# Performance work log

Hardware: AMD Instinct MI355X
Metric: run time of the kernel (lower is better)

Reference implementation:

```python
import jax, jax.numpy as jnp
import numpy as np

SEQ, BATCH = 256, 8
N_NODES = SEQ * BATCH
VOCAB, D_MODEL, H, D_K, D_FF, N_LAYERS, MAX_POS = 259, 256, 8, 32, 1024, 2, 128


def setup_inputs() -> dict:
    key = jax.random.key(0)
    ks = jax.random.split(key, 16)
    # structured causal edge list per sequence (dst attends to src <= dst, incl. self)
    tri_dst, tri_src = np.tril_indices(SEQ)
    offs = (np.arange(BATCH) * SEQ)[:, None]
    edge_src = jnp.asarray((tri_src[None, :] + offs).ravel(), dtype=jnp.int64)
    edge_dst = jnp.asarray((tri_dst[None, :] + offs).ravel(), dtype=jnp.int64)
    positions = jnp.tile(jnp.arange(SEQ, dtype=jnp.int64), BATCH)
    tokens = jax.random.randint(ks[0], (N_NODES,), 0, VOCAB, dtype=jnp.int64)
    s = 0.02
    p = lambda k, shp: jax.random.normal(k, shp, dtype=jnp.float32) * s
    return {
        "tokens": tokens, "positions": positions,
        "edge_src": edge_src, "edge_dst": edge_dst,
        "coord_emb": p(ks[1], (3, D_MODEL)),
        "pos_emb": p(ks[2], (MAX_POS, D_MODEL)),
        "value_emb": p(ks[3], (VOCAB, D_MODEL)),
        "ln1_scale": jnp.ones((N_LAYERS, D_MODEL)), "ln1_bias": jnp.zeros((N_LAYERS, D_MODEL)),
        "Wqkv": p(ks[4], (N_LAYERS, D_MODEL, 3 * D_MODEL)),
        "Wo": p(ks[5], (N_LAYERS, D_MODEL, D_MODEL)),
        "ln2_scale": jnp.ones((N_LAYERS, D_MODEL)), "ln2_bias": jnp.zeros((N_LAYERS, D_MODEL)),
        "W1": p(ks[6], (N_LAYERS, D_MODEL, D_FF)), "b1": jnp.zeros((N_LAYERS, D_FF)),
        "W2": p(ks[7], (N_LAYERS, D_FF, D_MODEL)), "b2": jnp.zeros((N_LAYERS, D_MODEL)),
        "lnf_scale": jnp.ones((D_MODEL,)), "lnf_bias": jnp.zeros((D_MODEL,)),
        "Wg": p(ks[8], (D_MODEL, VOCAB)), "bg": jnp.zeros((VOCAB,)),
    }


def _ln(x, scale, bias, eps=1e-5):
    mu = jnp.mean(x, axis=-1, keepdims=True)
    var = jnp.var(x, axis=-1, keepdims=True)
    return (x - mu) * jax.lax.rsqrt(var + eps) * scale + bias


def _graph_attention(x, src, dst, Wqkv, Wo, ln_s, ln_b):
    n = x.shape[0]
    xn = _ln(x, ln_s, ln_b)
    qkv = (xn @ Wqkv).reshape(n, 3, H, D_K)
    q, k, v = qkv[:, 0], qkv[:, 1], qkv[:, 2]  # [n, H, D_K] each
    # u_dot_v('k','q','score') per edge, scaled
    score = jnp.einsum("ehd,ehd->eh", k[src], q[dst]) / jnp.sqrt(jnp.float32(D_K))
    # edge_softmax over incoming edges of each dst node
    smax = jax.ops.segment_max(score, dst, num_segments=n)      # [n, H]
    ex = jnp.exp(score - smax[dst])                              # [E, H]
    denom = jax.ops.segment_sum(ex, dst, num_segments=n)        # [n, H]
    alpha = ex / denom[dst]
    # u_mul_e('v','softmax_score') + sum reduce -> z on dst nodes
    z = jax.ops.segment_sum(alpha[:, :, None] * v[src], dst, num_segments=n)  # [n, H, D_K]
    return x + z.reshape(n, D_MODEL) @ Wo


def reference(tokens, positions, edge_src, edge_dst, coord_emb, pos_emb, value_emb,
              ln1_scale, ln1_bias, Wqkv, Wo, ln2_scale, ln2_bias, W1, b1, W2, b2,
              lnf_scale, lnf_bias, Wg, bg):
    x = coord_emb[positions % 3] + pos_emb[positions // 3] + value_emb[tokens]
    for i in range(Wqkv.shape[0]):
        x = _graph_attention(x, edge_src, edge_dst, Wqkv[i], Wo[i], ln1_scale[i], ln1_bias[i])
        h = _ln(x, ln2_scale[i], ln2_bias[i])
        x = x + jax.nn.relu(h @ W1[i] + b1[i]) @ W2[i] + b2[i]
    out = _ln(x, lnf_scale, lnf_bias) @ Wg + bg
    return jax.nn.log_softmax(out, axis=-1)
```

## Files before the change

### kernel.cpp

```cpp
#include <hip/hip_runtime.h>
#include <hip/hip_bf16.h>

typedef __hip_bfloat16 bf16;
typedef unsigned short ushort_t;
typedef unsigned int uint_t;
typedef __attribute__((ext_vector_type(8))) short short8;
typedef __attribute__((ext_vector_type(4))) float floatx4;

#define D_MODEL 256
#define SEQ     256
#define BATCH   8
#define NN      2048
#define NHEAD   8
#define DK      32
#define DFF     1024
#define VOCAB   259
#define NLAYER  2

#define WQKVT_OFF 0
#define WOT_OFF   393216
#define W1T_OFF   524288
#define W2T_OFF   1048576
#define WGT_OFF   1572864
#define WT_TOTAL  1639168
#define LNP_TOTAL 2560
#define BP_TOTAL  2819

template<bool BF>
__device__ __forceinline__ float ldw(const void* p, int i) {
    if (BF) return __bfloat162float(((const bf16*)p)[i]);
    return ((const float*)p)[i];
}
template<bool BF>
__device__ __forceinline__ ushort_t ldb(const void* p, size_t i) {
    if (BF) return ((const ushort_t*)p)[i];
    bf16 h = __float2bfloat16(((const float*)p)[i]);
    ushort_t u; __builtin_memcpy(&u, &h, 2); return u;
}
template<bool I64>
__device__ __forceinline__ int ldi(const void* p, int i) {
    if (I64) return (int)(((const long long*)p)[i]);
    return ((const int*)p)[i];
}
__device__ __forceinline__ ushort_t f2bs(float f) {
    bf16 h = __float2bfloat16(f);
    ushort_t u; __builtin_memcpy(&u, &h, 2); return u;
}
__device__ __forceinline__ float bs2f(uint_t u16) {
    return __uint_as_float(u16 << 16);
}
__device__ __forceinline__ float wred_sum(float v) {
    #pragma unroll
    for (int m = 32; m > 0; m >>= 1) v += __shfl_xor(v, m, 64);
    return v;
}
__device__ __forceinline__ float wred_max(float v) {
    #pragma unroll
    for (int m = 32; m > 0; m >>= 1) v = fmaxf(v, __shfl_xor(v, m, 64));
    return v;
}
__device__ __forceinline__ bool detBF(const void* ln1s) {
    return *(const uint_t*)ln1s == 0x3F803F80u;
}
__device__ __forceinline__ bool detI64(const void* pos) {
    const int* p32 = (const int*)pos;
    return p32[1] == 0 && p32[2] == 1;
}

template<bool BF>
__device__ void ttile(const void* src, size_t srcOff, int K, int N, int tk, int tn,
                      ushort_t* dst, ushort_t (*tile)[68]) {
    int t = threadIdx.x;
    #pragma unroll
    for (int pass = 0; pass < 16; ++pass) {
        int e = pass * 256 + t;
        int kl = e >> 6, nl = e & 63;
        int n = tn * 64 + nl;
        tile[kl][nl] = (n < N) ? ldb<BF>(src, srcOff + (size_t)(tk*64 + kl) * N + n)
                               : (ushort_t)0;
    }
    __syncthreads();
    #pragma unroll
    for (int pass = 0; pass < 16; ++pass) {
        int e = pass * 256 + t;
        int nl = e >> 6, kl = e & 63;
        int n = tn * 64 + nl;
        if (n < N) dst[(size_t)n * K + tk*64 + kl] = tile[kl][nl];
    }
}

template<bool BF, bool I64>
__device__ void embedln16(const void* tok, const void* pos,
        const void* ce, const void* pe, const void* ve,
        const void* ln1s, const void* ln1b, int rowBase,
        float* x, ushort_t* xn) {
    int lane = threadIdx.x & 63, wave = threadIdx.x >> 6;
    #pragma unroll
    for (int i = 0; i < 4; ++i) {
        int n = rowBase + wave * 4 + i;
        int p  = ldi<I64>(pos, n);
        int tk = ldi<I64>(tok, n);
        int c0 = lane * 4;
        float v[4];
        #pragma unroll
        for (int j = 0; j < 4; ++j)
            v[j] = ldw<BF>(ce, (p % 3) * 256 + c0 + j)
                 + ldw<BF>(pe, (p / 3) * 256 + c0 + j)
                 + ldw<BF>(ve, tk * 256 + c0 + j);
        float s  = wred_sum(v[0] + v[1] + v[2] + v[3]);
        float s2 = wred_sum(v[0]*v[0] + v[1]*v[1] + v[2]*v[2] + v[3]*v[3]);
        float mu = s * (1.f/256.f);
        float var = s2 * (1.f/256.f) - mu * mu;
        float rstd = rsqrtf(var + 1e-5f);
        *reinterpret_cast<float4*>(&x[(size_t)n*256 + c0]) =
            make_float4(v[0], v[1], v[2], v[3]);
        ushort4 o;
        o.x = f2bs((v[0]-mu)*rstd*ldw<BF>(ln1s, c0+0) + ldw<BF>(ln1b, c0+0));
        o.y = f2bs((v[1]-mu)*rstd*ldw<BF>(ln1s, c0+1) + ldw<BF>(ln1b, c0+1));
        o.z = f2bs((v[2]-mu)*rstd*ldw<BF>(ln1s, c0+2) + ldw<BF>(ln1b, c0+2));
        o.w = f2bs((v[3]-mu)*rstd*ldw<BF>(ln1s, c0+3) + ldw<BF>(ln1b, c0+3));
        *reinterpret_cast<ushort4*>(&xn[(size_t)n*256 + c0]) = o;
    }
}

template<bool BF, bool I64>
__device__ void prep_body(const void* tok, const void* pos,
        const void* ce, const void* pe, const void* ve,
        const void* Wqkv, const void* Wo, const void* W1, const void* W2, const void* Wg,
        const void* ln1s, const void* ln1b, const void* ln2s, const void* ln2b,
        const void* lnfs, const void* lnfb,
        const void* b1, const void* b2, const void* bg,
        ushort_t* WT, float* lnP, float* bP, float* x, ushort_t* xn,
        ushort_t (*tile)[68]) {
    int blk = blockIdx.x;
    if (blk < 404) {
        const void* src; int K, N, tk, tn; size_t dstOff, srcOff;
        if (blk < 96)       { int L = blk/48, lo = blk%48; src=Wqkv; K=256; N=768;
                              srcOff=(size_t)L*196608; dstOff=WQKVT_OFF+(size_t)L*196608;
                              tk=lo/12; tn=lo%12; }
        else if (blk < 128) { int b2=blk-96, L=b2/16, lo=b2%16; src=Wo; K=256; N=256;
                              srcOff=(size_t)L*65536; dstOff=WOT_OFF+(size_t)L*65536;
                              tk=lo/4; tn=lo%4; }
        else if (blk < 256) { int b2=blk-128, L=b2/64, lo=b2%64; src=W1; K=256; N=1024;
                              srcOff=(size_t)L*262144; dstOff=W1T_OFF+(size_t)L*262144;
                              tk=lo/16; tn=lo%16; }
        else if (blk < 384) { int b2=blk-256, L=b2/64, lo=b2%64; src=W2; K=1024; N=256;
                              srcOff=(size_t)L*262144; dstOff=W2T_OFF+(size_t)L*262144;
                              tk=lo/4; tn=lo%4; }
        else                { int lo=blk-384; src=Wg; K=256; N=259;
                              srcOff=0; dstOff=WGT_OFF; tk=lo/5; tn=lo%5; }
        ttile<BF>(src, srcOff, K, N, tk, tn, WT + dstOff, tile);
    } else if (blk < 426) {
        int gid = (blk - 404) * 256 + threadIdx.x;
        if (gid < LNP_TOTAL) {
            float v;
            if      (gid < 512)  v = ldw<BF>(ln1s, gid);
            else if (gid < 1024) v = ldw<BF>(ln1b, gid - 512);
            else if (gid < 1536) v = ldw<BF>(ln2s, gid - 1024);
            else if (gid < 2048) v = ldw<BF>(ln2b, gid - 1536);
            else if (gid < 2304) v = ldw<BF>(lnfs, gid - 2048);
            else                 v = ldw<BF>(lnfb, gid - 2304);
            lnP[gid] = v;
        } else if (gid < LNP_TOTAL + BP_TOTAL) {
            int g = gid - LNP_TOTAL;
            float v;
            if      (g < 2048) v = ldw<BF>(b1, g);
            else if (g < 2560) v = ldw<BF>(b2, g - 2048);
            else               v = ldw<BF>(bg, g - 2560);
            bP[g] = v;
        }
    } else {
        embedln16<BF, I64>(tok, pos, ce, pe, ve, ln1s, ln1b, (blk - 426) * 16, x, xn);
    }
}

__global__ void __launch_bounds__(256) prep_k(const void* tok, const void* pos,
        const void* ce, const void* pe, const void* ve,
        const void* Wqkv, const void* Wo, const void* W1, const void* W2, const void* Wg,
        const void* ln1s, const void* ln1b, const void* ln2s, const void* ln2b,
        const void* lnfs, const void* lnfb,
        const void* b1, const void* b2, const void* bg,
        ushort_t* WT, float* lnP, float* bP, float* x, ushort_t* xn) {
    __shared__ ushort_t tile[64][68];
    bool BF = detBF(ln1s), I64 = detI64(pos);
    if (BF) { if (I64) prep_body<true,true >(tok,pos,ce,pe,ve,Wqkv,Wo,W1,W2,Wg,ln1s,ln1b,ln2s,ln2b,lnfs,lnfb,b1,b2,bg,WT,lnP,bP,x,xn,tile);
              else     prep_body<true,false>(tok,pos,ce,pe,ve,Wqkv,Wo,W1,W2,Wg,ln1s,ln1b,ln2s,ln2b,lnfs,lnfb,b1,b2,bg,WT,lnP,bP,x,xn,tile); }
    else    { if (I64) prep_body<false,true >(tok,pos,ce,pe,ve,Wqkv,Wo,W1,W2,Wg,ln1s,ln1b,ln2s,ln2b,lnfs,lnfb,b1,b2,bg,WT,lnP,bP,x,xn,tile);
              else     prep_body<false,false>(tok,pos,ce,pe,ve,Wqkv,Wo,W1,W2,Wg,ln1s,ln1b,ln2s,ln2b,lnfs,lnfb,b1,b2,bg,WT,lnP,bP,x,xn,tile); }
}

union AttnSH {
    struct {
        ushort_t Ks[SEQ][40];
        ushort_t Qs[64][40];
    } a;
    ushort_t Ps[64][264];
};
__global__ void __launch_bounds__(256) attn_k(const ushort_t* __restrict__ qkvB,
                                              ushort_t* __restrict__ zB) {
    __shared__ AttnSH u;
    __shared__ ushort_t Vt[32][264];
    int t = threadIdx.x;
    int lane = t & 63, wave = t >> 6;
    int quad = lane >> 4, l16 = lane & 15;
    int tile = blockIdx.x & 3, bh = blockIdx.x >> 2;
    int b = bh >> 3, h = bh & 7;
    int base = b * SEQ;
    int dstBase = tile * 64;
    int tileEnd = (tile + 1) * 64;

    int nV = tileEnd * 4;
    for (int i = t; i < nV; i += 256) {
        int src = i >> 2, g = i & 3;
        const ushort_t* rp = qkvB + (size_t)(base + src) * 768 + h * 32 + g * 8;
        uint4 kv = *reinterpret_cast<const uint4*>(rp + 256);
        *reinterpret_cast<uint4*>(&u.a.Ks[src][g * 8]) = kv;
        uint4 vv = *reinterpret_cast<const uint4*>(rp + 512);
        const ushort_t* vs = (const ushort_t*)&vv;
        #pragma unroll
        for (int j = 0; j < 8; ++j) Vt[g * 8 + j][src] = vs[j];
    }
    {
        int r = t >> 2, g = t & 3;
        uint4 qv = *reinterpret_cast<const uint4*>(
            qkvB + (size_t)(base + dstBase + r) * 768 + h * 32 + g * 8);
        *reinterpret_cast<uint4*>(&u.a.Qs[r][g * 8]) = qv;
    }
    __syncthreads();

    const float scale = 0.17677669529663687f;
    int stLim = tile * 4 + wave;
    int stCnt = stLim + 1;
    short8 qf = *reinterpret_cast<const short8*>(&u.a.Qs[wave * 16 + l16][quad * 8]);
    floatx4 accs[16];
    #pragma unroll
    for (int st = 0; st < 16; ++st) {
        if (st <= stLim) {
            short8 kf = *reinterpret_cast<const short8*>(&u.a.Ks[st * 16 + l16][quad * 8]);
            accs[st] = __builtin_amdgcn_mfma_f32_16x16x32_bf16(qf, kf, (floatx4){0.f,0.f,0.f,0.f}, 0, 0, 0);
        }
    }
    float mrow[4] = {-3e38f, -3e38f, -3e38f, -3e38f};
    #pragma unroll
    for (int st = 0; st < 16; ++st) {
        if (st <= stLim) {
            int srcg = st * 16 + l16;
            #pragma unroll
            for (int r = 0; r < 4; ++r) {
                int dstg = dstBase + wave * 16 + quad * 4 + r;
                float sv = (srcg <= dstg) ? accs[st][r] * scale : -3e38f;
                accs[st][r] = sv;
                mrow[r] = fmaxf(mrow[r], sv);
            }
        }
    }
    #pragma unroll
    for (int mk = 1; mk < 16; mk <<= 1)
        #pragma unroll
        for (int r = 0; r < 4; ++r) mrow[r] = fmaxf(mrow[r], __shfl_xor(mrow[r], mk, 64));
    float lrow[4] = {0.f, 0.f, 0.f, 0.f};
    #pragma unroll
    for (int st = 0; st < 16; ++st) {
        if (st <= stLim) {
            #pragma unroll
            for (int r = 0; r < 4; ++r) {
                float p = __expf(accs[st][r] - mrow[r]);
                accs[st][r] = p;
                lrow[r] += p;
            }
        }
    }
    #pragma unroll
    for (int mk = 1; mk < 16; mk <<= 1)
        #pragma unroll
        for (int r = 0; r < 4; ++r) lrow[r] += __shfl_xor(lrow[r], mk, 64);
    __syncthreads();

    #pragma unroll
    for (int st = 0; st < 16; ++st) {
        if (st <= stLim) {
            #pragma unroll
            for (int r = 0; r < 4; ++r)
                u.Ps[wave * 16 + quad * 4 + r][st * 16 + l16] = f2bs(accs[st][r]);
        }
    }
    if (stCnt & 1) {
        #pragma unroll
        for (int r = 0; r < 4; ++r)
            u.Ps[wave * 16 + quad * 4 + r][stCnt * 16 + l16] = 0;
    }
    __syncthreads();

    int ktCnt = (stCnt + 1) >> 1;
    floatx4 acco[2];
    acco[0] = (floatx4){0.f,0.f,0.f,0.f};
    acco[1] = (floatx4){0.f,0.f,0.f,0.f};
    #pragma unroll
    for (int kt = 0; kt < 8; ++kt) {
        if (kt < ktCnt) {
            short8 pf = *reinterpret_cast<const short8*>(&u.Ps[wave * 16 + l16][kt * 32 + quad * 8]);
            #pragma unroll
            for (int dn = 0; dn < 2; ++dn) {
                short8 vf = *reinterpret_cast<const short8*>(&Vt[dn * 16 + l16][kt * 32 + quad * 8]);
                acco[dn] = __builtin_amdgcn_mfma_f32_16x16x32_bf16(pf, vf, acco[dn], 0, 0, 0);
            }
        }
    }
    #pragma unroll
    for (int dn = 0; dn < 2; ++dn)
        #pragma unroll
        for (int r = 0; r < 4; ++r)
            zB[(size_t)(base + dstBase + wave * 16 + quad * 4 + r) * 256
               + h * 32 + dn * 16 + l16] = f2bs(acco[dn][r] / lrow[r]);
}

__global__ void __launch_bounds__(256) gemm_k(const ushort_t* __restrict__ A, int K,
        const ushort_t* __restrict__ BT, const float* __restrict__ bias,
        ushort_t* __restrict__ C, int ldc, int relu) {
    int t = threadIdx.x;
    int lane = t & 63, wave = t >> 6;
    int quad = lane >> 4, l16 = lane & 15;
    int wm = (wave >> 1) * 32, wn = (wave & 1) * 32;
    int rowBase = blockIdx.x * 64, colBase = blockIdx.y * 64;
    floatx4 acc[2][2];
    #pragma unroll
    for (int a = 0; a < 2; ++a)
        #pragma unroll
        for (int b = 0; b < 2; ++b) acc[a][b] = (floatx4){0.f,0.f,0.f,0.f};
    const ushort_t* a0 = A + (size_t)(rowBase + wm + l16) * K + quad * 8;
    const ushort_t* a1 = a0 + (size_t)16 * K;
    const ushort_t* b0 = BT + (size_t)(colBase + wn + l16) * K + quad * 8;
    const ushort_t* b1 = b0 + (size_t)16 * K;
    #pragma unroll 8
    for (int k0 = 0; k0 < K; k0 += 32) {
        short8 af0 = *reinterpret_cast<const short8*>(a0 + k0);
        short8 af1 = *reinterpret_cast<const short8*>(a1 + k0);
        short8 bf0 = *reinterpret_cast<const short8*>(b0 + k0);
        short8 bf1 = *reinterpret_cast<const short8*>(b1 + k0);
        acc[0][0] = __builtin_amdgcn_mfma_f32_16x16x32_bf16(af0, bf0, acc[0][0], 0,0,0);
        acc[0][1] = __builtin_amdgcn_mfma_f32_16x16x32_bf16(af0, bf1, acc[0][1], 0,0,0);
        acc[1][0] = __builtin_amdgcn_mfma_f32_16x16x32_bf16(af1, bf0, acc[1][0], 0,0,0);
        acc[1][1] = __builtin_amdgcn_mfma_f32_16x16x32_bf16(af1, bf1, acc[1][1], 0,0,0);
    }
    #pragma unroll
    for (int nt = 0; nt < 2; ++nt) {
        int col = colBase + wn + nt*16 + l16;
        float bb = bias ? bias[col] : 0.f;
        #pragma unroll
        for (int mt = 0; mt < 2; ++mt)
            #pragma unroll
            for (int r = 0; r < 4; ++r) {
                int row = rowBase + wm + mt*16 + quad*4 + r;
                float v = acc[mt][nt][r] + bb;
                if (relu) v = fmaxf(v, 0.f);
                C[(size_t)row * ldc + col] = f2bs(v);
            }
    }
}

__global__ void __launch_bounds__(256) gemmresln_k(const ushort_t* __restrict__ A, int K,
        const ushort_t* __restrict__ BT, const float* __restrict__ bias,
        float* __restrict__ x, const float* __restrict__ ls, const float* __restrict__ lb,
        ushort_t* __restrict__ xnG,
        const void* __restrict__ ln1sRaw, const ushort_t* __restrict__ WgT,
        const float* __restrict__ bgP, void* __restrict__ outp, int doLogits) {
    __shared__ float sparts[4][16][256];
    __shared__ ushort_t xnS[16][264];
    float (*Lg)[273] = reinterpret_cast<float (*)[273]>(&sparts[1][0][0]);
    int t = threadIdx.x;
    int lane = t & 63, wave = t >> 6;
    int quad = lane >> 4, l16 = lane & 15;
    int rowBase = blockIdx.x * 16;
    int Kq = K >> 2;
    int wk0 = wave * Kq;

    {
        floatx4 acc[16];
        #pragma unroll
        for (int nt = 0; nt < 16; ++nt) acc[nt] = (floatx4){0.f,0.f,0.f,0.f};
        const ushort_t* a0 = A + (size_t)(rowBase + l16) * K + wk0 + quad * 8;
        for (int k0 = 0; k0 < Kq; k0 += 32) {
            short8 af = *reinterpret_cast<const short8*>(a0 + k0);
            #pragma unroll
            for (int nt = 0; nt < 16; ++nt) {
                short8 bv = *reinterpret_cast<const short8*>(
                    BT + (size_t)(nt*16 + l16) * K + wk0 + k0 + quad * 8);
                acc[nt] = __builtin_amdgcn_mfma_f32_16x16x32_bf16(af, bv, acc[nt], 0,0,0);
            }
        }
        #pragma unroll
        for (int nt = 0; nt < 16; ++nt)
            #pragma unroll
            for (int r = 0; r < 4; ++r)
                sparts[wave][quad*4 + r][nt*16 + l16] = acc[nt][r];
    }
    __syncthreads();
    {
        float* flat0 = &sparts[0][0][0];
        #pragma unroll
        for (int i = 0; i < 16; ++i) {
            int idx = i * 256 + t;
            int row = idx >> 8, col = idx & 255;
            float v = flat0[idx] + (&sparts[1][0][0])[idx]
                    + (&sparts[2][0][0])[idx] + (&sparts[3][0][0])[idx];
            if (bias) v += bias[col];
            v += x[(size_t)(rowBase + row) * 256 + col];
            x[(size_t)(rowBase + row) * 256 + col] = v;
            flat0[idx] = v;
        }
    }
    __syncthreads();
    #pragma unroll
    for (int i = 0; i < 4; ++i) {
        int row = wave*4 + i;
        int c0 = lane * 4;
        float4 vv = *reinterpret_cast<const float4*>(&sparts[0][row][c0]);
        float s  = wred_sum(vv.x + vv.y + vv.z + vv.w);
        float s2 = wred_sum(vv.x*vv.x + vv.y*vv.y + vv.z*vv.z + vv.w*vv.w);
        float mu = s * (1.f/256.f);
        float var = s2 * (1.f/256.f) - mu*mu;
        float rstd = rsqrtf(var + 1e-5f);
        ushort4 o;
        o.x = f2bs((vv.x-mu)*rstd*ls[c0+0] + lb[c0+0]);
        o.y = f2bs((vv.y-mu)*rstd*ls[c0+1] + lb[c0+1]);
        o.z = f2bs((vv.z-mu)*rstd*ls[c0+2] + lb[c0+2]);
        o.w = f2bs((vv.w-mu)*rstd*ls[c0+3] + lb[c0+3]);
        *reinterpret_cast<ushort4*>(&xnG[(size_t)(rowBase+row)*256 + c0]) = o;
        if (doLogits) *reinterpret_cast<ushort4*>(&xnS[row][c0]) = o;
    }
    if (!doLogits) return;
    __syncthreads();
    int cb = wave * 64;
    const ushort_t* a0 = &xnS[l16][quad * 8];
    {
        floatx4 acc[4];
        #pragma unroll
        for (int nt = 0; nt < 4; ++nt) acc[nt] = (floatx4){0.f,0.f,0.f,0.f};
        #pragma unroll
        for (int kc = 0; kc < 8; ++kc) {
            short8 af = *reinterpret_cast<const short8*>(a0 + kc * 32);
            #pragma unroll
            for (int nt = 0; nt < 4; ++nt) {
                short8 bv = *reinterpret_cast<const short8*>(
                    WgT + (size_t)(cb + nt*16 + l16) * 256 + kc*32 + quad*8);
                acc[nt] = __builtin_amdgcn_mfma_f32_16x16x32_bf16(af, bv, acc[nt], 0,0,0);
            }
        }
        __syncthreads();
        #pragma unroll
        for (int nt = 0; nt < 4; ++nt) {
            int col = cb + nt*16 + l16;
            float bb = bgP[col];
            #pragma unroll
            for (int r = 0; r < 4; ++r)
                Lg[quad*4 + r][col] = acc[nt][r] + bb;
        }
    }
    if (wave == 0) {
        floatx4 acc = (floatx4){0.f,0.f,0.f,0.f};
        int n = 256 + l16;
        int nc = (n < VOCAB) ? n : 0;
        const ushort_t* b0 = WgT + (size_t)nc * 256 + quad * 8;
        #pragma unroll
        for (int kc = 0; kc < 8; ++kc) {
            short8 af = *reinterpret_cast<const short8*>(a0 + kc * 32);
            short8 bv = *reinterpret_cast<const short8*>(b0 + kc * 32);
            acc = __builtin_amdgcn_mfma_f32_16x16x32_bf16(af, bv, acc, 0,0,0);
        }
        #pragma unroll
        for (int r = 0; r < 4; ++r)
            Lg[quad*4 + r][256 + l16] = (n < VOCAB) ? (acc[r] + bgP[n]) : -1e30f;
    }
    __syncthreads();
    int outBF = detBF(ln1sRaw) ? 1 : 0;
    #pragma unroll
    for (int i = 0; i < 4; ++i) {
        int row = wave*4 + i;
        float v0 = Lg[row][lane],     v1 = Lg[row][lane+64];
        float v2 = Lg[row][lane+128], v3 = Lg[row][lane+192];
        float v4 = (lane < 16) ? Lg[row][256+lane] : -1e30f;
        float m = wred_max(fmaxf(fmaxf(fmaxf(v0,v1), fmaxf(v2,v3)), v4));
        float se = __expf(v0-m) + __expf(v1-m) + __expf(v2-m) + __expf(v3-m)
                 + ((lane < 16) ? __expf(v4-m) : 0.f);
        se = wred_sum(se);
        float lse = m + logf(se);
        size_t nbase = (size_t)(rowBase + row) * VOCAB;
        if (outBF) {
            ushort_t* o = (ushort_t*)outp + nbase;
            o[lane]     = f2bs(v0 - lse);
            o[lane+64]  = f2bs(v1 - lse);
            o[lane+128] = f2bs(v2 - lse);
            o[lane+192] = f2bs(v3 - lse);
            if (lane < 3) o[256+lane] = f2bs(v4 - lse);
        } else {
            float* o = (float*)outp + nbase;
            o[lane]     = v0 - lse;
            o[lane+64]  = v1 - lse;
            o[lane+128] = v2 - lse;
            o[lane+192] = v3 - lse;
            if (lane < 3) o[256+lane] = v4 - lse;
        }
    }
}

extern "C" void kernel_launch(void* const* d_in, const int* in_sizes, int n_in,
                              void* d_out, int out_size, void* d_ws, size_t ws_size,
                              hipStream_t stream) {
    const void* tok  = d_in[0];
    const void* pos  = d_in[1];
    const void* ce   = d_in[4];
    const void* pe   = d_in[5];
    const void* ve   = d_in[6];
    const void* ln1s = d_in[7];
    const void* ln1b = d_in[8];
    const void* Wqkv = d_in[9];
    const void* Wo   = d_in[10];
    const void* ln2s = d_in[11];
    const void* ln2b = d_in[12];
    const void* W1   = d_in[13];
    const void* b1   = d_in[14];
    const void* W2   = d_in[15];
    const void* b2   = d_in[16];
    const void* lnfs = d_in[17];
    const void* lnfb = d_in[18];
    const void* Wg   = d_in[19];
    const void* bg   = d_in[20];

    char* base = (char*)d_ws;
    float*    lnP  = (float*)base;
    float*    bP   = (float*)(base + 10240);
    float*    x    = (float*)(base + 22528);
    ushort_t* xn   = (ushort_t*)(base + 2119680);
    ushort_t* zB   = (ushort_t*)(base + 3168256);
    ushort_t* ffB  = (ushort_t*)(base + 4216832);
    ushort_t* WT   = (ushort_t*)(base + 8411136);
    ushort_t* qkvB = (ushort_t*)(base + 11689472);

    prep_k<<<554, 256, 0, stream>>>(tok, pos, ce, pe, ve,
        Wqkv, Wo, W1, W2, Wg, ln1s, ln1b, ln2s, ln2b, lnfs, lnfb,
        b1, b2, bg, WT, lnP, bP, x, xn);
    for (int L = 0; L < NLAYER; ++L) {
        gemm_k<<<dim3(32, 12), 256, 0, stream>>>(xn, 256,
            WT + WQKVT_OFF + (size_t)L * 768 * 256, nullptr, qkvB, 768, 0);
        attn_k<<<256, 256, 0, stream>>>(qkvB, zB);
        gemmresln_k<<<128, 256, 0, stream>>>(zB, 256,
            WT + WOT_OFF + (size_t)L * 256 * 256, nullptr,
            x, lnP + 1024 + L * 256, lnP + 1536 + L * 256, xn,
            ln1s, WT + WGT_OFF, bP + 2560, d_out, 0);
        gemm_k<<<dim3(32, 16), 256, 0, stream>>>(xn, 256,
            WT + W1T_OFF + (size_t)L * 1024 * 256, bP + L * 1024, ffB, 1024, 1);
        const float* lsN = (L == 0) ? (lnP + 256)       : (lnP + 2048);
        const float* lbN = (L == 0) ? (lnP + 512 + 256) : (lnP + 2304);
        gemmresln_k<<<128, 256, 0, stream>>>(ffB, 1024,
            WT + W2T_OFF + (size_t)L * 256 * 1024, bP + 2048 + L * 256,
            x, lsN, lbN, xn,
            ln1s, WT + WGT_OFF, bP + 2560, d_out, (L == NLAYER - 1) ? 1 : 0);
    }
}
```

Before: 239.3 us.

## Fuse all stages into a cooperative persistent megakernel with grid syncs

After: 241.6 us. No clear change (+0.9%).

```diff
diff --git a/kernel.cpp b/kernel.cpp
--- a/kernel.cpp
+++ b/kernel.cpp
@@ -1,5 +1,8 @@
 #include <hip/hip_runtime.h>
 #include <hip/hip_bf16.h>
+#include <hip/hip_cooperative_groups.h>
+
+namespace cg = cooperative_groups;
 
 typedef __hip_bfloat16 bf16;
 typedef unsigned short ushort_t;
@@ -26,6 +29,10 @@
 #define LNP_TOTAL 2560
 #define BP_TOTAL  2819
 
+__device__ __forceinline__ ushort_t f2bs(float f) {
+    bf16 h = __float2bfloat16(f);
+    ushort_t u; __builtin_memcpy(&u, &h, 2); return u;
+}
 template<bool BF>
 __device__ __forceinline__ float ldw(const void* p, int i) {
     if (BF) return __bfloat162float(((const bf16*)p)[i]);
@@ -34,20 +41,21 @@
 template<bool BF>
 __device__ __forceinline__ ushort_t ldb(const void* p, size_t i) {
     if (BF) return ((const ushort_t*)p)[i];
-    bf16 h = __float2bfloat16(((const float*)p)[i]);
-    ushort_t u; __builtin_memcpy(&u, &h, 2); return u;
+    return f2bs(((const float*)p)[i]);
 }
 template<bool I64>
 __device__ __forceinline__ int ldi(const void* p, int i) {
     if (I64) return (int)(((const long long*)p)[i]);
     return ((const int*)p)[i];
 }
-__device__ __forceinline__ ushort_t f2bs(float f) {
-    bf16 h = __float2bfloat16(f);
-    ushort_t u; __builtin_memcpy(&u, &h, 2); return u;
-}
-__device__ __forceinline__ float bs2f(uint_t u16) {
-    return __uint_as_float(u16 << 16);
+__device__ __forceinline__ float ldwr(const void* p, int i, bool BF) {
+    return BF ? __bfloat162float(((const bf16*)p)[i]) : ((const float*)p)[i];
+}
+__device__ __forceinline__ ushort_t ldbr(const void* p, size_t i, bool BF) {
+    return BF ? ((const ushort_t*)p)[i] : f2bs(((const float*)p)[i]);
+}
+__device__ __forceinline__ int ldir(const void* p, int i, bool I64) {
+    return I64 ? (int)(((const long long*)p)[i]) : ((const int*)p)[i];
 }
 __device__ __forceinline__ float wred_sum(float v) {
     #pragma unroll
@@ -65,6 +73,332 @@
 __device__ __forceinline__ bool detI64(const void* pos) {
     const int* p32 = (const int*)pos;
     return p32[1] == 0 && p32[2] == 1;
+}
+
+union AttnSH {
+    struct {
+        ushort_t Ks[SEQ][40];
+        ushort_t Qs[64][40];
+    } a;
+    ushort_t Ps[64][264];
+};
+
+__device__ void attn_body(const ushort_t* __restrict__ qkvB,
+                          ushort_t* __restrict__ zB, int task,
+                          AttnSH& u, ushort_t (*Vt)[264]) {
+    int t = threadIdx.x;
+    int lane = t & 63, wave = t >> 6;
+    int quad = lane >> 4, l16 = lane & 15;
+    int tile = task & 3, bh = task >> 2;
+    int b = bh >> 3, h = bh & 7;
+    int base = b * SEQ;
+    int dstBase = tile * 64;
+    int tileEnd = (tile + 1) * 64;
+
+    int nV = tileEnd * 4;
+    for (int i = t; i < nV; i += 256) {
+        int src = i >> 2, g = i & 3;
+        const ushort_t* rp = qkvB + (size_t)(base + src) * 768 + h * 32 + g * 8;
+        uint4 kv = *reinterpret_cast<const uint4*>(rp + 256);
+        *reinterpret_cast<uint4*>(&u.a.Ks[src][g * 8]) = kv;
+        uint4 vv = *reinterpret_cast<const uint4*>(rp + 512);
+        const ushort_t* vs = (const ushort_t*)&vv;
+        #pragma unroll
+        for (int j = 0; j < 8; ++j) Vt[g * 8 + j][src] = vs[j];
+    }
+    {
+        int r = t >> 2, g = t & 3;
+        uint4 qv = *reinterpret_cast<const uint4*>(
+            qkvB + (size_t)(base + dstBase + r) * 768 + h * 32 + g * 8);
+        *reinterpret_cast<uint4*>(&u.a.Qs[r][g * 8]) = qv;
+    }
+    __syncthreads();
+
+    const float scale = 0.17677669529663687f;
+    int stLim = tile * 4 + wave;
+    int stCnt = stLim + 1;
+    short8 qf = *reinterpret_cast<const short8*>(&u.a.Qs[wave * 16 + l16][quad * 8]);
+    floatx4 accs[16];
+    #pragma unroll
+    for (int st = 0; st < 16; ++st) {
+        if (st <= stLim) {
+            short8 kf = *reinterpret_cast<const short8*>(&u.a.Ks[st * 16 + l16][quad * 8]);
+            accs[st] = __builtin_amdgcn_mfma_f32_16x16x32_bf16(qf, kf, (floatx4){0.f,0.f,0.f,0.f}, 0, 0, 0);
+        }
+    }
+    float mrow[4] = {-3e38f, -3e38f, -3e38f, -3e38f};
+    #pragma unroll
+    for (int st = 0; st < 16; ++st) {
+        if (st <= stLim) {
+            int srcg = st * 16 + l16;
+            #pragma unroll
+            for (int r = 0; r < 4; ++r) {
+                int dstg = dstBase + wave * 16 + quad * 4 + r;
+                float sv = (srcg <= dstg) ? accs[st][r] * scale : -3e38f;
+                accs[st][r] = sv;
+                mrow[r] = fmaxf(mrow[r], sv);
+            }
+        }
+    }
+    #pragma unroll
+    for (int mk = 1; mk < 16; mk <<= 1)
+        #pragma unroll
+        for (int r = 0; r < 4; ++r) mrow[r] = fmaxf(mrow[r], __shfl_xor(mrow[r], mk, 64));
+    float lrow[4] = {0.f, 0.f, 0.f, 0.f};
+    #pragma unroll
+    for (int st = 0; st < 16; ++st) {
+        if (st <= stLim) {
+            #pragma unroll
+            for (int r = 0; r < 4; ++r) {
+                float p = __expf(accs[st][r] - mrow[r]);
+                accs[st][r] = p;
+                lrow[r] += p;
+            }
+        }
+    }
+    #pragma unroll
+    for (int mk = 1; mk < 16; mk <<= 1)
+        #pragma unroll
+        for (int r = 0; r < 4; ++r) lrow[r] += __shfl_xor(lrow[r], mk, 64);
+    __syncthreads();
+
+    #pragma unroll
+    for (int st = 0; st < 16; ++st) {
+        if (st <= stLim) {
+            #pragma unroll
+            for (int r = 0; r < 4; ++r)
+                u.Ps[wave * 16 + quad * 4 + r][st * 16 + l16] = f2bs(accs[st][r]);
+        }
+    }
+    if (stCnt & 1) {
+        #pragma unroll
+        for (int r = 0; r < 4; ++r)
+            u.Ps[wave * 16 + quad * 4 + r][stCnt * 16 + l16] = 0;
+    }
+    __syncthreads();
+
+    int ktCnt = (stCnt + 1) >> 1;
+    floatx4 acco[2];
+    acco[0] = (floatx4){0.f,0.f,0.f,0.f};
+    acco[1] = (floatx4){0.f,0.f,0.f,0.f};
+    #pragma unroll
+    for (int kt = 0; kt < 8; ++kt) {
+        if (kt < ktCnt) {
+            short8 pf = *reinterpret_cast<const short8*>(&u.Ps[wave * 16 + l16][kt * 32 + quad * 8]);
+            #pragma unroll
+            for (int dn = 0; dn < 2; ++dn) {
+                short8 vf = *reinterpret_cast<const short8*>(&Vt[dn * 16 + l16][kt * 32 + quad * 8]);
+                acco[dn] = __builtin_amdgcn_mfma_f32_16x16x32_bf16(pf, vf, acco[dn], 0, 0, 0);
+            }
+        }
+    }
+    #pragma unroll
+    for (int dn = 0; dn < 2; ++dn)
+        #pragma unroll
+        for (int r = 0; r < 4; ++r)
+            zB[(size_t)(base + dstBase + wave * 16 + quad * 4 + r) * 256
+               + h * 32 + dn * 16 + l16] = f2bs(acco[dn][r] / lrow[r]);
+}
+
+__global__ void __launch_bounds__(256) attn_k(const ushort_t* __restrict__ qkvB,
+                                              ushort_t* __restrict__ zB) {
+    __shared__ AttnSH u;
+    __shared__ ushort_t Vt[32][264];
+    attn_body(qkvB, zB, blockIdx.x, u, Vt);
+}
+
+__device__ void gemm64_body(const ushort_t* __restrict__ A, int K,
+        const ushort_t* __restrict__ BT, const float* __restrict__ bias,
+        ushort_t* __restrict__ C, int ldc, int relu, int rowBase, int colBase) {
+    int t = threadIdx.x;
+    int lane = t & 63, wave = t >> 6;
+    int quad = lane >> 4, l16 = lane & 15;
+    int wm = (wave >> 1) * 32, wn = (wave & 1) * 32;
+    floatx4 acc[2][2];
+    #pragma unroll
+    for (int a = 0; a < 2; ++a)
+        #pragma unroll
+        for (int b = 0; b < 2; ++b) acc[a][b] = (floatx4){0.f,0.f,0.f,0.f};
+    const ushort_t* a0 = A + (size_t)(rowBase + wm + l16) * K + quad * 8;
+    const ushort_t* a1 = a0 + (size_t)16 * K;
+    const ushort_t* b0 = BT + (size_t)(colBase + wn + l16) * K + quad * 8;
+    const ushort_t* b1 = b0 + (size_t)16 * K;
+    #pragma unroll 8
+    for (int k0 = 0; k0 < K; k0 += 32) {
+        short8 af0 = *reinterpret_cast<const short8*>(a0 + k0);
+        short8 af1 = *reinterpret_cast<const short8*>(a1 + k0);
+        short8 bf0 = *reinterpret_cast<const short8*>(b0 + k0);
+        short8 bf1 = *reinterpret_cast<const short8*>(b1 + k0);
+        acc[0][0] = __builtin_amdgcn_mfma_f32_16x16x32_bf16(af0, bf0, acc[0][0], 0,0,0);
+        acc[0][1] = __builtin_amdgcn_mfma_f32_16x16x32_bf16(af0, bf1, acc[0][1], 0,0,0);
+        acc[1][0] = __builtin_amdgcn_mfma_f32_16x16x32_bf16(af1, bf0, acc[1][0], 0,0,0);
+        acc[1][1] = __builtin_amdgcn_mfma_f32_16x16x32_bf16(af1, bf1, acc[1][1], 0,0,0);
+    }
+    #pragma unroll
+    for (int nt = 0; nt < 2; ++nt) {
+        int col = colBase + wn + nt*16 + l16;
+        float bb = bias ? bias[col] : 0.f;
+        #pragma unroll
+        for (int mt = 0; mt < 2; ++mt)
+            #pragma unroll
+            for (int r = 0; r < 4; ++r) {
+                int row = rowBase + wm + mt*16 + quad*4 + r;
+                float v = acc[mt][nt][r] + bb;
+                if (relu) v = fmaxf(v, 0.f);
+                C[(size_t)row * ldc + col] = f2bs(v);
+            }
+    }
+}
+
+__global__ void __launch_bounds__(256) gemm_k(const ushort_t* __restrict__ A, int K,
+        const ushort_t* __restrict__ BT, const float* __restrict__ bias,
+        ushort_t* __restrict__ C, int ldc, int relu) {
+    gemm64_body(A, K, BT, bias, C, ldc, relu, blockIdx.x * 64, blockIdx.y * 64);
+}
+
+__global__ void __launch_bounds__(256) gemmresln_k(const ushort_t* __restrict__ A, int K,
+        const ushort_t* __restrict__ BT, const float* __restrict__ bias,
+        float* __restrict__ x, const float* __restrict__ ls, const float* __restrict__ lb,
+        ushort_t* __restrict__ xnG,
+        const void* __restrict__ ln1sRaw, const ushort_t* __restrict__ WgT,
+        const float* __restrict__ bgP, void* __restrict__ outp, int doLogits) {
+    __shared__ float sparts[4][16][256];
+    __shared__ ushort_t xnS[16][264];
+    float (*Lg)[273] = reinterpret_cast<float (*)[273]>(&sparts[1][0][0]);
+    int t = threadIdx.x;
+    int lane = t & 63, wave = t >> 6;
+    int quad = lane >> 4, l16 = lane & 15;
+    int rowBase = blockIdx.x * 16;
+    int Kq = K >> 2;
+    int wk0 = wave * Kq;
+
+    {
+        floatx4 acc[16];
+        #pragma unroll
+        for (int nt = 0; nt < 16; ++nt) acc[nt] = (floatx4){0.f,0.f,0.f,0.f};
+        const ushort_t* a0 = A + (size_t)(rowBase + l16) * K + wk0 + quad * 8;
+        for (int k0 = 0; k0 < Kq; k0 += 32) {
+            short8 af = *reinterpret_cast<const short8*>(a0 + k0);
+            #pragma unroll
+            for (int nt = 0; nt < 16; ++nt) {
+                short8 bv = *reinterpret_cast<const short8*>(
+                    BT + (size_t)(nt*16 + l16) * K + wk0 + k0 + quad * 8);
+                acc[nt] = __builtin_amdgcn_mfma_f32_16x16x32_bf16(af, bv, acc[nt], 0,0,0);
+            }
+        }
+        #pragma unroll
+        for (int nt = 0; nt < 16; ++nt)
+            #pragma unroll
+            for (int r = 0; r < 4; ++r)
+                sparts[wave][quad*4 + r][nt*16 + l16] = acc[nt][r];
+    }
+    __syncthreads();
+    {
+        float* flat0 = &sparts[0][0][0];
+        #pragma unroll
+        for (int i = 0; i < 16; ++i) {
+            int idx = i * 256 + t;
+            int row = idx >> 8, col = idx & 255;
+            float v = flat0[idx] + (&sparts[1][0][0])[idx]
+                    + (&sparts[2][0][0])[idx] + (&sparts[3][0][0])[idx];
+            if (bias) v += bias[col];
+            v += x[(size_t)(rowBase + row) * 256 + col];
+            x[(size_t)(rowBase + row) * 256 + col] = v;
+            flat0[idx] = v;
+        }
+    }
+    __syncthreads();
+    #pragma unroll
+    for (int i = 0; i < 4; ++i) {
+        int row = wave*4 + i;
+        int c0 = lane * 4;
+        float4 vv = *reinterpret_cast<const float4*>(&sparts[0][row][c0]);
+        float s  = wred_sum(vv.x + vv.y + vv.z + vv.w);
+        float s2 = wred_sum(vv.x*vv.x + vv.y*vv.y + vv.z*vv.z + vv.w*vv.w);
+        float mu = s * (1.f/256.f);
+        float var = s2 * (1.f/256.f) - mu*mu;
+        float rstd = rsqrtf(var + 1e-5f);
+        ushort4 o;
+        o.x = f2bs((vv.x-mu)*rstd*ls[c0+0] + lb[c0+0]);
+        o.y = f2bs((vv.y-mu)*rstd*ls[c0+1] + lb[c0+1]);
+        o.z = f2bs((vv.z-mu)*rstd*ls[c0+2] + lb[c0+2]);
+        o.w = f2bs((vv.w-mu)*rstd*ls[c0+3] + lb[c0+3]);
+        *reinterpret_cast<ushort4*>(&xnG[(size_t)(rowBase+row)*256 + c0]) = o;
+        if (doLogits) *reinterpret_cast<ushort4*>(&xnS[row][c0]) = o;
+    }
+    if (!doLogits) return;
+    __syncthreads();
+    int cb = wave * 64;
+    const ushort_t* a0 = &xnS[l16][quad * 8];
+    {
+        floatx4 acc[4];
+        #pragma unroll
+        for (int nt = 0; nt < 4; ++nt) acc[nt] = (floatx4){0.f,0.f,0.f,0.f};
+        #pragma unroll
+        for (int kc = 0; kc < 8; ++kc) {
+            short8 af = *reinterpret_cast<const short8*>(a0 + kc * 32);
+            #pragma unroll
+            for (int nt = 0; nt < 4; ++nt) {
+                short8 bv = *reinterpret_cast<const short8*>(
+                    WgT + (size_t)(cb + nt*16 + l16) * 256 + kc*32 + quad*8);
+                acc[nt] = __builtin_amdgcn_mfma_f32_16x16x32_bf16(af, bv, acc[nt], 0,0,0);
+            }
+        }
+        __syncthreads();
+        #pragma unroll
+        for (int nt = 0; nt < 4; ++nt) {
+            int col = cb + nt*16 + l16;
+            float bb = bgP[col];
+            #pragma unroll
+            for (int r = 0; r < 4; ++r)
+                Lg[quad*4 + r][col] = acc[nt][r] + bb;
+        }
+    }
+    if (wave == 0) {
+        floatx4 acc = (floatx4){0.f,0.f,0.f,0.f};
+        int n = 256 + l16;
+        int nc = (n < VOCAB) ? n : 0;
+        const ushort_t* b0 = WgT + (size_t)nc * 256 + quad * 8;
+        #pragma unroll
+        for (int kc = 0; kc < 8; ++kc) {
+            short8 af = *reinterpret_cast<const short8*>(a0 + kc * 32);
+            short8 bv = *reinterpret_cast<const short8*>(b0 + kc * 32);
+            acc = __builtin_amdgcn_mfma_f32_16x16x32_bf16(af, bv, acc, 0,0,0);
+        }
+        #pragma unroll
+        for (int r = 0; r < 4; ++r)
+            Lg[quad*4 + r][256 + l16] = (n < VOCAB) ? (acc[r] + bgP[n]) : -1e30f;
+    }
+    __syncthreads();
+    int outBF = detBF(ln1sRaw) ? 1 : 0;
+    #pragma unroll
+    for (int i = 0; i < 4; ++i) {
+        int row = wave*4 + i;
+        float v0 = Lg[row][lane],     v1 = Lg[row][lane+64];
+        float v2 = Lg[row][lane+128], v3 = Lg[row][lane+192];
+        float v4 = (lane < 16) ? Lg[row][256+lane] : -1e30f;
+        float m = wred_max(fmaxf(fmaxf(fmaxf(v0,v1), fmaxf(v2,v3)), v4));
+        float se = __expf(v0-m) + __expf(v1-m) + __expf(v2-m) + __expf(v3-m)
+                 + ((lane < 16) ? __expf(v4-m) : 0.f);
+        se = wred_sum(se);
+        float lse = m + logf(se);
+        size_t nbase = (size_t)(rowBase + row) * VOCAB;
+        if (outBF) {
+            ushort_t* o = (ushort_t*)outp + nbase;
+            o[lane]     = f2bs(v0 - lse);
+            o[lane+64]  = f2bs(v1 - lse);
+            o[lane+128] = f2bs(v2 - lse);
+            o[lane+192] = f2bs(v3 - lse);
+            if (lane < 3) o[256+lane] = f2bs(v4 - lse);
+        } else {
+            float* o = (float*)outp + nbase;
+            o[lane]     = v0 - lse;
+            o[lane+64]  = v1 - lse;
+            o[lane+128] = v2 - lse;
+            o[lane+192] = v3 - lse;
+            if (lane < 3) o[256+lane] = v4 - lse;
+        }
+    }
 }
 
 template<bool BF>
@@ -189,232 +523,145 @@
               else     prep_body<false,false>(tok,pos,ce,pe,ve,Wqkv,Wo,W1,W2,Wg,ln1s,ln1b,ln2s,ln2b,lnfs,lnfb,b1,b2,bg,WT,lnP,bP,x,xn,tile); }
 }
 
-union AttnSH {
-    struct {
-        ushort_t Ks[SEQ][40];
-        ushort_t Qs[64][40];
-    } a;
-    ushort_t Ps[64][264];
+struct MegaP {
+    const void *tok, *pos, *ce, *pe, *ve;
+    const void *Wqkv, *Wo, *W1, *W2, *Wg;
+    const void *ln1s, *ln1b, *ln2s, *ln2b, *lnfs, *lnfb, *b1, *b2, *bg;
+    ushort_t* WT; float* lnP; float* bP; float* x; ushort_t* xn;
+    ushort_t* zB; ushort_t* qkvB; void* outp;
 };
-__global__ void __launch_bounds__(256) attn_k(const ushort_t* __restrict__ qkvB,
-                                              ushort_t* __restrict__ zB) {
-    __shared__ AttnSH u;
-    __shared__ ushort_t Vt[32][264];
+
+union __align__(16) MegaSH {
+    ushort_t tile[64][68];
+    struct { AttnSH u; ushort_t Vt[32][264]; } at;
+    struct { ushort_t hmid[16][1032]; float xrow[16][256]; } ff;
+    struct { float xrow[16][256]; } wo;
+    struct { float Lg[16][273]; } lg;
+};
+
+__device__ void prep_task(int task, const MegaP& p, ushort_t (*tile)[68],
+                          bool BF, bool I64) {
     int t = threadIdx.x;
-    int lane = t & 63, wave = t >> 6;
+    if (task < 404) {
+        const void* src; int K, N, tk, tn; size_t dstOff, srcOff;
+        if (task < 96)       { int L = task/48, lo = task%48; src=p.Wqkv; K=256; N=768;
+                               srcOff=(size_t)L*196608; dstOff=WQKVT_OFF+(size_t)L*196608;
+                               tk=lo/12; tn=lo%12; }
+        else if (task < 128) { int b2=task-96, L=b2/16, lo=b2%16; src=p.Wo; K=256; N=256;
+                               srcOff=(size_t)L*65536; dstOff=WOT_OFF+(size_t)L*65536;
+                               tk=lo/4; tn=lo%4; }
+        else if (task < 256) { int b2=task-128, L=b2/64, lo=b2%64; src=p.W1; K=256; N=1024;
+                               srcOff=(size_t)L*262144; dstOff=W1T_OFF+(size_t)L*262144;
+                               tk=lo/16; tn=lo%16; }
+        else if (task < 384) { int b2=task-256, L=b2/64, lo=b2%64; src=p.W2; K=1024; N=256;
+                               srcOff=(size_t)L*262144; dstOff=W2T_OFF+(size_t)L*262144;
+                               tk=lo/4; tn=lo%4; }
+        else                 { int lo=task-384; src=p.Wg; K=256; N=259;
+                               srcOff=0; dstOff=WGT_OFF; tk=lo/5; tn=lo%5; }
+        ushort_t* dst = p.WT + dstOff;
+        #pragma unroll
+        for (int pass = 0; pass < 16; ++pass) {
+            int e = pass * 256 + t;
+            int kl = e >> 6, nl = e & 63;
+            int n = tn * 64 + nl;
+            tile[kl][nl] = (n < N) ? ldbr(src, srcOff + (size_t)(tk*64 + kl) * N + n, BF)
+                                   : (ushort_t)0;
+        }
+        __syncthreads();
+        #pragma unroll
+        for (int pass = 0; pass < 16; ++pass) {
+            int e = pass * 256 + t;
+            int nl = e >> 6, kl = e & 63;
+            int n = tn * 64 + nl;
+            if (n < N) dst[(size_t)n * K + tk*64 + kl] = tile[kl][nl];
+        }
+    } else if (task < 426) {
+        int gid = (task - 404) * 256 + t;
+        if (gid < LNP_TOTAL) {
+            float v;
+            if      (gid < 512)  v = ldwr(p.ln1s, gid, BF);
+            else if (gid < 1024) v = ldwr(p.ln1b, gid - 512, BF);
+            else if (gid < 1536) v = ldwr(p.ln2s, gid - 1024, BF);
+            else if (gid < 2048) v = ldwr(p.ln2b, gid - 1536, BF);
+            else if (gid < 2304) v = ldwr(p.lnfs, gid - 2048, BF);
+            else                 v = ldwr(p.lnfb, gid - 2304, BF);
+            p.lnP[gid] = v;
+        } else if (gid < LNP_TOTAL + BP_TOTAL) {
+            int g = gid - LNP_TOTAL;
+            float v;
+            if      (g < 2048) v = ldwr(p.b1, g, BF);
+            else if (g < 2560) v = ldwr(p.b2, g - 2048, BF);
+            else               v = ldwr(p.bg, g - 2560, BF);
+            p.bP[g] = v;
+        }
+    } else {
+        int lane = t & 63, wave = t >> 6;
+        int rowBase = (task - 426) * 16;
+        #pragma unroll
+        for (int i = 0; i < 4; ++i) {
+            int n = rowBase + wave * 4 + i;
+            int pp = ldir(p.pos, n, I64);
+            int tk = ldir(p.tok, n, I64);
+            int c0 = lane * 4;
+            float v[4];
+            #pragma unroll
+            for (int j = 0; j < 4; ++j)
+                v[j] = ldwr(p.ce, (pp % 3) * 256 + c0 + j, BF)
+                     + ldwr(p.pe, (pp / 3) * 256 + c0 + j, BF)
+                     + ldwr(p.ve, tk * 256 + c0 + j, BF);
+            float s  = wred_sum(v[0] + v[1] + v[2] + v[3]);
+            float s2 = wred_sum(v[0]*v[0] + v[1]*v[1] + v[2]*v[2] + v[3]*v[3]);
+            float mu = s * (1.f/256.f);
+            float var = s2 * (1.f/256.f) - mu * mu;
+            float rstd = rsqrtf(var + 1e-5f);
+            *reinterpret_cast<float4*>(&p.x[(size_t)n*256 + c0]) =
+                make_float4(v[0], v[1], v[2], v[3]);
+            ushort4 o;
+            o.x = f2bs((v[0]-mu)*rstd*ldwr(p.ln1s, c0+0, BF) + ldwr(p.ln1b, c0+0, BF));
+            o.y = f2bs((v[1]-mu)*rstd*ldwr(p.ln1s, c0+1, BF) + ldwr(p.ln1b, c0+1, BF));
+            o.z = f2bs((v[2]-mu)*rstd*ldwr(p.ln1s, c0+2, BF) + ldwr(p.ln1b, c0+2, BF));
+            o.w = f2bs((v[3]-mu)*rstd*ldwr(p.ln1s, c0+3, BF) + ldwr(p.ln1b, c0+3, BF));
+            *reinterpret_cast<ushort4*>(&p.xn[(size_t)n*256 + c0]) = o;
+        }
+    }
+}
+
+__device__ void wo_body(const ushort_t* __restrict__ A, const ushort_t* __restrict__ BT,
+        float* __restrict__ x, const float* ls, const float* lb,
+        ushort_t* __restrict__ xnG, int rowBase, float (*xrow)[256]) {
+    int t = threadIdx.x, lane = t & 63, wave = t >> 6;
     int quad = lane >> 4, l16 = lane & 15;
-    int tile = blockIdx.x & 3, bh = blockIdx.x >> 2;
-    int b = bh >> 3, h = bh & 7;
-    int base = b * SEQ;
-    int dstBase = tile * 64;
-    int tileEnd = (tile + 1) * 64;
-
-    int nV = tileEnd * 4;
-    for (int i = t; i < nV; i += 256) {
-        int src = i >> 2, g = i & 3;
-        const ushort_t* rp = qkvB + (size_t)(base + src) * 768 + h * 32 + g * 8;
-        uint4 kv = *reinterpret_cast<const uint4*>(rp + 256);
-        *reinterpret_cast<uint4*>(&u.a.Ks[src][g * 8]) = kv;
-        uint4 vv = *reinterpret_cast<const uint4*>(rp + 512);
-        const ushort_t* vs = (const ushort_t*)&vv;
-        #pragma unroll
-        for (int j = 0; j < 8; ++j) Vt[g * 8 + j][src] = vs[j];
-    }
-    {
-        int r = t >> 2, g = t & 3;
-        uint4 qv = *reinterpret_cast<const uint4*>(
-            qkvB + (size_t)(base + dstBase + r) * 768 + h * 32 + g * 8);
-        *reinterpret_cast<uint4*>(&u.a.Qs[r][g * 8]) = qv;
-    }
-    __syncthreads();
-
-    const float scale = 0.17677669529663687f;
-    int stLim = tile * 4 + wave;
-    int stCnt = stLim + 1;
-    short8 qf = *reinterpret_cast<const short8*>(&u.a.Qs[wave * 16 + l16][quad * 8]);
-    floatx4 accs[16];
-    #pragma unroll
-    for (int st = 0; st < 16; ++st) {
-        if (st <= stLim) {
-            short8 kf = *reinterpret_cast<const short8*>(&u.a.Ks[st * 16 + l16][quad * 8]);
-            accs[st] = __builtin_amdgcn_mfma_f32_16x16x32_bf16(qf, kf, (floatx4){0.f,0.f,0.f,0.f}, 0, 0, 0);
-        }
-    }
-    float mrow[4] = {-3e38f, -3e38f, -3e38f, -3e38f};
-    #pragma unroll
-    for (int st = 0; st < 16; ++st) {
-        if (st <= stLim) {
-            int srcg = st * 16 + l16;
-            #pragma unroll
-            for (int r = 0; r < 4; ++r) {
-                int dstg = dstBase + wave * 16 + quad * 4 + r;
-                float sv = (srcg <= dstg) ? accs[st][r] * scale : -3e38f;
-                accs[st][r] = sv;
-                mrow[r] = fmaxf(mrow[r], sv);
-            }
-        }
-    }
-    #pragma unroll
-    for (int mk = 1; mk < 16; mk <<= 1)
-        #pragma unroll
-        for (int r = 0; r < 4; ++r) mrow[r] = fmaxf(mrow[r], __shfl_xor(mrow[r], mk, 64));
-    float lrow[4] = {0.f, 0.f, 0.f, 0.f};
-    #pragma unroll
-    for (int st = 0; st < 16; ++st) {
-        if (st <= stLim) {
-            #pragma unroll
-            for (int r = 0; r < 4; ++r) {
-                float p = __expf(accs[st][r] - mrow[r]);
-                accs[st][r] = p;
-                lrow[r] += p;
-            }
-        }
-    }
-    #pragma unroll
-    for (int mk = 1; mk < 16; mk <<= 1)
-        #pragma unroll
-        for (int r = 0; r < 4; ++r) lrow[r] += __shfl_xor(lrow[r], mk, 64);
-    __syncthreads();
-
-    #pragma unroll
-    for (int st = 0; st < 16; ++st) {
-        if (st <= stLim) {
-            #pragma unroll
-            for (int r = 0; r < 4; ++r)
-                u.Ps[wave * 16 + quad * 4 + r][st * 16 + l16] = f2bs(accs[st][r]);
-        }
-    }
-    if (stCnt & 1) {
-        #pragma unroll
-        for (int r = 0; r < 4; ++r)
-            u.Ps[wave * 16 + quad * 4 + r][stCnt * 16 + l16] = 0;
-    }
-    __syncthreads();
-
-    int ktCnt = (stCnt + 1) >> 1;
-    floatx4 acco[2];
-    acco[0] = (floatx4){0.f,0.f,0.f,0.f};
-    acco[1] = (floatx4){0.f,0.f,0.f,0.f};
-    #pragma unroll
-    for (int kt = 0; kt < 8; ++kt) {
-        if (kt < ktCnt) {
-            short8 pf = *reinterpret_cast<const short8*>(&u.Ps[wave * 16 + l16][kt * 32 + quad * 8]);
-            #pragma unroll
-            for (int dn = 0; dn < 2; ++dn) {
-                short8 vf = *reinterpret_cast<const short8*>(&Vt[dn * 16 + l16][kt * 32 + quad * 8]);
-                acco[dn] = __builtin_amdgcn_mfma_f32_16x16x32_bf16(pf, vf, acco[dn], 0, 0, 0);
-            }
-        }
-    }
-    #pragma unroll
-    for (int dn = 0; dn < 2; ++dn)
-        #pragma unroll
-        for (int r = 0; r < 4; ++r)
-            zB[(size_t)(base + dstBase + wave * 16 + quad * 4 + r) * 256
-               + h * 32 + dn * 16 + l16] = f2bs(acco[dn][r] / lrow[r]);
-}
-
-__global__ void __launch_bounds__(256) gemm_k(const ushort_t* __restrict__ A, int K,
-        const ushort_t* __restrict__ BT, const float* __restrict__ bias,
-        ushort_t* __restrict__ C, int ldc, int relu) {
-    int t = threadIdx.x;
-    int lane = t & 63, wave = t >> 6;
-    int quad = lane >> 4, l16 = lane & 15;
-    int wm = (wave >> 1) * 32, wn = (wave & 1) * 32;
-    int rowBase = blockIdx.x * 64, colBase = blockIdx.y * 64;
-    floatx4 acc[2][2];
-    #pragma unroll
-    for (int a = 0; a < 2; ++a)
-        #pragma unroll
-        for (int b = 0; b < 2; ++b) acc[a][b] = (floatx4){0.f,0.f,0.f,0.f};
-    const ushort_t* a0 = A + (size_t)(rowBase + wm + l16) * K + quad * 8;
-    const ushort_t* a1 = a0 + (size_t)16 * K;
-    const ushort_t* b0 = BT + (size_t)(colBase + wn + l16) * K + quad * 8;
-    const ushort_t* b1 = b0 + (size_t)16 * K;
-    #pragma unroll 8
-    for (int k0 = 0; k0 < K; k0 += 32) {
-        short8 af0 = *reinterpret_cast<const short8*>(a0 + k0);
-        short8 af1 = *reinterpret_cast<const short8*>(a1 + k0);
-        short8 bf0 = *reinterpret_cast<const short8*>(b0 + k0);
-        short8 bf1 = *reinterpret_cast<const short8*>(b1 + k0);
-        acc[0][0] = __builtin_amdgcn_mfma_f32_16x16x32_bf16(af0, bf0, acc[0][0], 0,0,0);
-        acc[0][1] = __builtin_amdgcn_mfma_f32_16x16x32_bf16(af0, bf1, acc[0][1], 0,0,0);
-        acc[1][0] = __builtin_amdgcn_mfma_f32_16x16x32_bf16(af1, bf0, acc[1][0], 0,0,0);
-        acc[1][1] = __builtin_amdgcn_mfma_f32_16x16x32_bf16(af1, bf1, acc[1][1], 0,0,0);
-    }
-    #pragma unroll
-    for (int nt = 0; nt < 2; ++nt) {
-        int col = colBase + wn + nt*16 + l16;
-        float bb = bias ? bias[col] : 0.f;
-        #pragma unroll
-        for (int mt = 0; mt < 2; ++mt)
-            #pragma unroll
-            for (int r = 0; r < 4; ++r) {
-                int row = rowBase + wm + mt*16 + quad*4 + r;
-                float v = acc[mt][nt][r] + bb;
-                if (relu) v = fmaxf(v, 0.f);
-                C[(size_t)row * ldc + col] = f2bs(v);
-            }
-    }
-}
-
-__global__ void __launch_bounds__(256) gemmresln_k(const ushort_t* __restrict__ A, int K,
-        const ushort_t* __restrict__ BT, const float* __restrict__ bias,
-        float* __restrict__ x, const float* __restrict__ ls, const float* __restrict__ lb,
-        ushort_t* __restrict__ xnG,
-        const void* __restrict__ ln1sRaw, const ushort_t* __restrict__ WgT,
-        const float* __restrict__ bgP, void* __restrict__ outp, int doLogits) {
-    __shared__ float sparts[4][16][256];
-    __shared__ ushort_t xnS[16][264];
-    float (*Lg)[273] = reinterpret_cast<float (*)[273]>(&sparts[1][0][0]);
-    int t = threadIdx.x;
-    int lane = t & 63, wave = t >> 6;
-    int quad = lane >> 4, l16 = lane & 15;
-    int rowBase = blockIdx.x * 16;
-    int Kq = K >> 2;
-    int wk0 = wave * Kq;
-
-    {
-        floatx4 acc[16];
-        #pragma unroll
-        for (int nt = 0; nt < 16; ++nt) acc[nt] = (floatx4){0.f,0.f,0.f,0.f};
-        const ushort_t* a0 = A + (size_t)(rowBase + l16) * K + wk0 + quad * 8;
-        for (int k0 = 0; k0 < Kq; k0 += 32) {
-            short8 af = *reinterpret_cast<const short8*>(a0 + k0);
-            #pragma unroll
-            for (int nt = 0; nt < 16; ++nt) {
-                short8 bv = *reinterpret_cast<const short8*>(
-                    BT + (size_t)(nt*16 + l16) * K + wk0 + k0 + quad * 8);
-                acc[nt] = __builtin_amdgcn_mfma_f32_16x16x32_bf16(af, bv, acc[nt], 0,0,0);
-            }
-        }
-        #pragma unroll
-        for (int nt = 0; nt < 16; ++nt)
-            #pragma unroll
-            for (int r = 0; r < 4; ++r)
-                sparts[wave][quad*4 + r][nt*16 + l16] = acc[nt][r];
-    }
-    __syncthreads();
-    {
-        float* flat0 = &sparts[0][0][0];
-        #pragma unroll
-        for (int i = 0; i < 16; ++i) {
-            int idx = i * 256 + t;
-            int row = idx >> 8, col = idx & 255;
-            float v = flat0[idx] + (&sparts[1][0][0])[idx]
-                    + (&sparts[2][0][0])[idx] + (&sparts[3][0][0])[idx];
-            if (bias) v += bias[col];
-            v += x[(size_t)(rowBase + row) * 256 + col];
+    int cb = wave * 64;
+    floatx4 acc[4];
+    #pragma unroll
+    for (int nt = 0; nt < 4; ++nt) acc[nt] = (floatx4){0.f,0.f,0.f,0.f};
+    const ushort_t* a0 = A + (size_t)(rowBase + l16) * 256 + quad * 8;
+    #pragma unroll
+    for (int k0 = 0; k0 < 256; k0 += 32) {
+        short8 af = *reinterpret_cast<const short8*>(a0 + k0);
+        #pragma unroll
+        for (int nt = 0; nt < 4; ++nt) {
+            short8 bv = *reinterpret_cast<const short8*>(
+                BT + (size_t)(cb + nt*16 + l16) * 256 + k0 + quad * 8);
+            acc[nt] = __builtin_amdgcn_mfma_f32_16x16x32_bf16(af, bv, acc[nt], 0,0,0);
+        }
+    }
+    #pragma unroll
+    for (int nt = 0; nt < 4; ++nt) {
+        int col = cb + nt*16 + l16;
+        #pragma unroll
+        for (int r = 0; r < 4; ++r) {
+            int row = quad*4 + r;
+            float v = acc[nt][r] + x[(size_t)(rowBase + row) * 256 + col];
             x[(size_t)(rowBase + row) * 256 + col] = v;
-            flat0[idx] = v;
+            xrow[row][col] = v;
         }
     }
     __syncthreads();
     #pragma unroll
     for (int i = 0; i < 4; ++i) {
-        int row = wave*4 + i;
-        int c0 = lane * 4;
-        float4 vv = *reinterpret_cast<const float4*>(&sparts[0][row][c0]);
+        int row = wave*4 + i, c0 = lane * 4;
+        float4 vv = *reinterpret_cast<const float4*>(&xrow[row][c0]);
         float s  = wred_sum(vv.x + vv.y + vv.z + vv.w);
         float s2 = wred_sum(vv.x*vv.x + vv.y*vv.y + vv.z*vv.z + vv.w*vv.w);
         float mu = s * (1.f/256.f);
@@ -426,12 +673,95 @@
         o.z = f2bs((vv.z-mu)*rstd*ls[c0+2] + lb[c0+2]);
         o.w = f2bs((vv.w-mu)*rstd*ls[c0+3] + lb[c0+3]);
         *reinterpret_cast<ushort4*>(&xnG[(size_t)(rowBase+row)*256 + c0]) = o;
-        if (doLogits) *reinterpret_cast<ushort4*>(&xnS[row][c0]) = o;
-    }
-    if (!doLogits) return;
-    __syncthreads();
+    }
+}
+
+__device__ void ff_body(const ushort_t* xnIO, const ushort_t* __restrict__ W1T,
+        const float* __restrict__ b1P, const ushort_t* __restrict__ W2T,
+        const float* __restrict__ b2P, float* __restrict__ x,
+        const float* ls, const float* lb, int rowBase,
+        ushort_t (*hmid)[1032], float (*xrow)[256]) {
+    int t = threadIdx.x, lane = t & 63, wave = t >> 6;
+    int quad = lane >> 4, l16 = lane & 15;
+    {
+        floatx4 acc[16];
+        #pragma unroll
+        for (int nt = 0; nt < 16; ++nt) acc[nt] = (floatx4){0.f,0.f,0.f,0.f};
+        const ushort_t* a0 = xnIO + (size_t)(rowBase + l16) * 256 + quad * 8;
+        #pragma unroll
+        for (int k0 = 0; k0 < 256; k0 += 32) {
+            short8 af = *reinterpret_cast<const short8*>(a0 + k0);
+            #pragma unroll
+            for (int nt = 0; nt < 16; ++nt) {
+                short8 bv = *reinterpret_cast<const short8*>(
+                    W1T + (size_t)(wave*256 + nt*16 + l16) * 256 + k0 + quad * 8);
+                acc[nt] = __builtin_amdgcn_mfma_f32_16x16x32_bf16(af, bv, acc[nt], 0,0,0);
+            }
+        }
+        #pragma unroll
+        for (int nt = 0; nt < 16; ++nt) {
+            int col = wave*256 + nt*16 + l16;
+            float bb = b1P[col];
+            #pragma unroll
+            for (int r = 0; r < 4; ++r)
+                hmid[quad*4 + r][col] = f2bs(fmaxf(acc[nt][r] + bb, 0.f));
+        }
+    }
+    __syncthreads();
+    {
+        floatx4 acc[4];
+        #pragma unroll
+        for (int nt = 0; nt < 4; ++nt) acc[nt] = (floatx4){0.f,0.f,0.f,0.f};
+        #pragma unroll 8
+        for (int k0 = 0; k0 < 1024; k0 += 32) {
+            short8 af = *reinterpret_cast<const short8*>(&hmid[l16][k0 + quad * 8]);
+            #pragma unroll
+            for (int nt = 0; nt < 4; ++nt) {
+                short8 bv = *reinterpret_cast<const short8*>(
+                    W2T + (size_t)(wave*64 + nt*16 + l16) * 1024 + k0 + quad * 8);
+                acc[nt] = __builtin_amdgcn_mfma_f32_16x16x32_bf16(af, bv, acc[nt], 0,0,0);
+            }
+        }
+        #pragma unroll
+        for (int nt = 0; nt < 4; ++nt) {
+            int col = wave*64 + nt*16 + l16;
+            float bb = b2P[col];
+            #pragma unroll
+            for (int r = 0; r < 4; ++r) {
+                int row = quad*4 + r;
+                float v = acc[nt][r] + bb + x[(size_t)(rowBase + row) * 256 + col];
+                x[(size_t)(rowBase + row) * 256 + col] = v;
+                xrow[row][col] = v;
+            }
+        }
+    }
+    __syncthreads();
+    ushort_t* xnOut = const_cast<ushort_t*>(xnIO);
+    #pragma unroll
+    for (int i = 0; i < 4; ++i) {
+        int row = wave*4 + i, c0 = lane * 4;
+        float4 vv = *reinterpret_cast<const float4*>(&xrow[row][c0]);
+        float s  = wred_sum(vv.x + vv.y + vv.z + vv.w);
+        float s2 = wred_sum(vv.x*vv.x + vv.y*vv.y + vv.z*vv.z + vv.w*vv.w);
+        float mu = s * (1.f/256.f);
+        float var = s2 * (1.f/256.f) - mu*mu;
+        float rstd = rsqrtf(var + 1e-5f);
+        ushort4 o;
+        o.x = f2bs((vv.x-mu)*rstd*ls[c0+0] + lb[c0+0]);
+        o.y = f2bs((vv.y-mu)*rstd*ls[c0+1] + lb[c0+1]);
+        o.z = f2bs((vv.z-mu)*rstd*ls[c0+2] + lb[c0+2]);
+        o.w = f2bs((vv.w-mu)*rstd*ls[c0+3] + lb[c0+3]);
+        *reinterpret_cast<ushort4*>(&xnOut[(size_t)(rowBase+row)*256 + c0]) = o;
+    }
+}
+
+__device__ void logits_body(const ushort_t* __restrict__ xnG,
+        const ushort_t* __restrict__ WgT, const float* __restrict__ bgP,
+        void* __restrict__ outp, int outBF, int rowBase, float (*Lg)[273]) {
+    int t = threadIdx.x, lane = t & 63, wave = t >> 6;
+    int quad = lane >> 4, l16 = lane & 15;
+    const ushort_t* a0 = xnG + (size_t)(rowBase + l16) * 256 + quad * 8;
     int cb = wave * 64;
-    const ushort_t* a0 = &xnS[l16][quad * 8];
     {
         floatx4 acc[4];
         #pragma unroll
@@ -446,7 +776,6 @@
                 acc[nt] = __builtin_amdgcn_mfma_f32_16x16x32_bf16(af, bv, acc[nt], 0,0,0);
             }
         }
-        __syncthreads();
         #pragma unroll
         for (int nt = 0; nt < 4; ++nt) {
             int col = cb + nt*16 + l16;
@@ -472,7 +801,6 @@
             Lg[quad*4 + r][256 + l16] = (n < VOCAB) ? (acc[r] + bgP[n]) : -1e30f;
     }
     __syncthreads();
-    int outBF = detBF(ln1sRaw) ? 1 : 0;
     #pragma unroll
     for (int i = 0; i < 4; ++i) {
         int row = wave*4 + i;
@@ -503,6 +831,59 @@
     }
 }
 
+__global__ void __launch_bounds__(256, 2) mega_k(MegaP p) {
+    __shared__ MegaSH sh;
+    cg::grid_group grid = cg::this_grid();
+    bool BF = detBF(p.ln1s), I64 = detI64(p.pos);
+    int nb = gridDim.x;
+
+    for (int task = blockIdx.x; task < 554; task += nb) {
+        prep_task(task, p, sh.tile, BF, I64);
+        __syncthreads();
+    }
+    grid.sync();
+
+    for (int L = 0; L < NLAYER; ++L) {
+        const ushort_t* WqkvT = p.WT + WQKVT_OFF + (size_t)L * 196608;
+        for (int task = blockIdx.x; task < 384; task += nb)
+            gemm64_body(p.xn, 256, WqkvT, nullptr, p.qkvB, 768, 0,
+                        (task & 31) * 64, (task >> 5) * 64);
+        grid.sync();
+
+        for (int task = blockIdx.x; task < 256; task += nb) {
+            attn_body(p.qkvB, p.zB, task, sh.at.u, sh.at.Vt);
+            __syncthreads();
+        }
+        grid.sync();
+
+        const ushort_t* WoT = p.WT + WOT_OFF + (size_t)L * 65536;
+        for (int task = blockIdx.x; task < 128; task += nb) {
+            wo_body(p.zB, WoT, p.x, p.lnP + 1024 + L * 256, p.lnP + 1536 + L * 256,
+                    p.xn, task * 16, sh.wo.xrow);
+            __syncthreads();
+        }
+        grid.sync();
+
+        const ushort_t* W1T = p.WT + W1T_OFF + (size_t)L * 262144;
+        const ushort_t* W2T = p.WT + W2T_OFF + (size_t)L * 262144;
+        const float* lsN = (L == 0) ? (p.lnP + 256) : (p.lnP + 2048);
+        const float* lbN = (L == 0) ? (p.lnP + 768) : (p.lnP + 2304);
+        for (int task = blockIdx.x; task < 128; task += nb) {
+            ff_body(p.xn, W1T, p.bP + L * 1024, W2T, p.bP + 2048 + L * 256,
+                    p.x, lsN, lbN, task * 16, sh.ff.hmid, sh.ff.xrow);
+            __syncthreads();
+        }
+        grid.sync();
+    }
+
+    int outBF = BF ? 1 : 0;
+    for (int task = blockIdx.x; task < 128; task += nb) {
+        logits_body(p.xn, p.WT + WGT_OFF, p.bP + 2560, p.outp, outBF,
+                    task * 16, sh.lg.Lg);
+        __syncthreads();
+    }
+}
+
 extern "C" void kernel_launch(void* const* d_in, const int* in_sizes, int n_in,
                               void* d_out, int out_size, void* d_ws, size_t ws_size,
                               hipStream_t stream) {
@@ -536,6 +917,43 @@
     ushort_t* WT   = (ushort_t*)(base + 8411136);
     ushort_t* qkvB = (ushort_t*)(base + 11689472);
 
+    static int megaGrid = -1;
+    if (megaGrid < 0) {
+        int dev = 0;
+        (void)hipGetDevice(&dev);
+        int coop = 0;
+        (void)hipDeviceGetAttribute(&coop, hipDeviceAttributeCooperativeLaunch, dev);
+        if (!coop) {
+            megaGrid = 0;
+        } else {
+            int nCU = 0;
+            if (hipDeviceGetAttribute(&nCU, hipDeviceAttributeMultiprocessorCount, dev)
+                    != hipSuccess || nCU <= 0) nCU = 256;
+            int mb = 0;
+            if (hipOccupancyMaxActiveBlocksPerMultiprocessor(&mb, mega_k, 256, 0)
+                    != hipSuccess || mb < 1) mb = 1;
+            long g = (long)nCU * (mb >= 2 ? 2 : 1);
+            if (g > 512) g = 512;
+            if (g < 64)  g = 64;
+            megaGrid = (int)g;
+        }
+    }
+
+    if (megaGrid > 0) {
+        MegaP mp;
+        mp.tok = tok;  mp.pos = pos;  mp.ce = ce;  mp.pe = pe;  mp.ve = ve;
+        mp.Wqkv = Wqkv; mp.Wo = Wo;  mp.W1 = W1;  mp.W2 = W2;  mp.Wg = Wg;
+        mp.ln1s = ln1s; mp.ln1b = ln1b; mp.ln2s = ln2s; mp.ln2b = ln2b;
+        mp.lnfs = lnfs; mp.lnfb = lnfb; mp.b1 = b1; mp.b2 = b2; mp.bg = bg;
+        mp.WT = WT; mp.lnP = lnP; mp.bP = bP; mp.x = x; mp.xn = xn;
+        mp.zB = zB; mp.qkvB = qkvB; mp.outp = d_out;
+        void* args[] = { &mp };
+        hipError_t e = hipLaunchCooperativeKernel((const void*)mega_k,
+                dim3(megaGrid), dim3(256), args, 0, stream);
+        if (e == hipSuccess) return;
+        megaGrid = 0;
+    }
+
     prep_k<<<554, 256, 0, stream>>>(tok, pos, ce, pe, ve,
         Wqkv, Wo, W1, W2, Wg, ln1s, ln1b, ln2s, ln2b, lnfs, lnfb,
         b1, b2, bg, WT, lnP, bP, x, xn);
```
